# Optimization experiments

Measured on AMD Instinct MI355X. Metric: run time of the kernel, lower is better.

## Reference

```python
import jax, jax.numpy as jnp
import numpy as np

F = 32          # fmap_size = (256 // 16) * 2
WIN = F // 8 - 1  # window = 3
HID = 160
HID4 = 640
N = 4096
Q = 16


def setup_inputs() -> dict:
    key = jax.random.key(0)
    ks = jax.random.split(key, 24)

    def lin(k, i, o):
        return jax.random.normal(k, (i, o), jnp.float32) * (1.0 / np.sqrt(i))

    return {
        "feature_pos": jax.random.normal(ks[0], (N, Q, HID), jnp.float32),
        "query_embedding": jax.random.normal(ks[1], (N, Q, HID), jnp.float32),
        "attn_matrix": jax.random.normal(ks[2], (N, Q, F * F), jnp.float32),
        "ws1": lin(ks[3], HID, HID4), "bs1": jnp.zeros((HID4,), jnp.float32),
        "ws2": lin(ks[4], HID4, HID4), "bs2": jnp.zeros((HID4,), jnp.float32),
        "ws3": lin(ks[5], HID4, HID4), "bs3": jnp.zeros((HID4,), jnp.float32),
        "ws4": lin(ks[6], HID4, 1), "bs4": jnp.zeros((1,), jnp.float32),
        "wp1": lin(ks[7], HID, HID4), "bp1": jnp.zeros((HID4,), jnp.float32),
        "wp2": lin(ks[8], HID4, HID4), "bp2": jnp.zeros((HID4,), jnp.float32),
        "wp3": lin(ks[9], HID4, HID4), "bp3": jnp.zeros((HID4,), jnp.float32),
        "wp4": lin(ks[10], HID4, 4), "bp4": jnp.zeros((4,), jnp.float32),
    }


def _mlp(x, w1, b1, w2, b2, w3, b3, w4, b4):
    h = jax.nn.relu(x @ w1 + b1)
    h = jax.nn.relu(h @ w2 + b2)
    h = jax.nn.relu(h @ w3 + b3)
    return h @ w4 + b4


def _gauss_blur3(x):
    # torchvision GaussianBlur(3, sigma=1.0): separable 3-tap, reflect padding
    e = np.exp(-0.5)
    k = jnp.asarray([e, 1.0, e], jnp.float32) / np.float32(1.0 + 2.0 * e)
    xp = jnp.pad(x, ((0, 0), (1, 1), (0, 0)), mode="reflect")
    x = k[0] * xp[:, :-2] + k[1] * xp[:, 1:-1] + k[2] * xp[:, 2:]
    xp = jnp.pad(x, ((0, 0), (0, 0), (1, 1)), mode="reflect")
    return k[0] * xp[:, :, :-2] + k[1] * xp[:, :, 1:-1] + k[2] * xp[:, :, 2:]


def _process_attnmap(am):
    # am: [N, F, F]
    n = am.shape[0]
    ab = _gauss_blur3(am)
    ab = (ab - ab.mean(axis=(1, 2), keepdims=True)) / jnp.std(ab, axis=(1, 2), keepdims=True, ddof=1)
    idx = jnp.argmax(ab.reshape(n, -1), axis=1)
    px = (idx % F).astype(jnp.int32)
    py = (idx // F).astype(jnp.int32)
    # vectorized windowed mean of clamped sigmoid (masked instead of per-sample slicing)
    s = jnp.clip(jax.nn.sigmoid(am), 1e-4, 1.0 - 1e-4)
    pos = jnp.arange(F)
    colmask = ((pos[None, :] >= jnp.maximum(0, px - WIN)[:, None]) &
               (pos[None, :] < jnp.minimum(F, px + WIN)[:, None])).astype(s.dtype)  # [N,F]
    rowmask = ((pos[None, :] >= jnp.maximum(0, py - WIN)[:, None]) &
               (pos[None, :] < jnp.minimum(F, py + WIN)[:, None])).astype(s.dtype)
    colsum = s.sum(axis=1)  # [N,F] sum over rows -> per-column totals
    rowsum = s.sum(axis=2)  # [N,F] sum over cols -> per-row totals
    tempx = (colsum * colmask).sum(axis=1) / (F * colmask.sum(axis=1))
    tempy = (rowsum * rowmask).sum(axis=1) / (F * rowmask.sum(axis=1))
    prepos = jnp.stack([px, py], axis=1).astype(jnp.float32)          # [N,2]
    presize = jnp.stack([tempx, tempy], axis=1) * np.float32(F)        # [N,2]
    return prepos, presize


def reference(feature_pos, query_embedding, attn_matrix,
              ws1, bs1, ws2, bs2, ws3, bs3, ws4, bs4,
              wp1, bp1, wp2, bp2, wp3, bp3, wp4, bp4):
    n = query_embedding.shape[0]
    qe = query_embedding.mean(axis=1)   # [N, HID]
    fp = feature_pos.mean(axis=1)       # [N, HID]
    am = attn_matrix.mean(axis=1).reshape(n, F, F)
    score = _mlp(qe, ws1, bs1, ws2, bs2, ws3, bs3, ws4, bs4).reshape(n)
    bbox_info = _mlp(fp, wp1, bp1, wp2, bp2, wp3, bp3, wp4, bp4)  # [N,4]
    sizeoffset = jnp.clip(bbox_info[:, :2], -2.0, 2.0)
    posoffset = jnp.clip(bbox_info[:, 2:], -2.0, 2.0)
    prepos, presize = _process_attnmap(am)
    xy = (prepos + posoffset) / np.float32(F)
    wh = (presize + sizeoffset) / np.float32(F)
    xy = xy - 0.5 * wh  # predict_center
    bbox = jnp.concatenate([xy, wh], axis=1)
    return bbox, score
```

## Files before the change

kernel.cpp:

```cpp
#include <hip/hip_runtime.h>
#include <hip/hip_bf16.h>
#include <stdint.h>

#define HID 160
#define HID4 640
#define FDIM 32
#define NPIX 1024

#define GK0 0.27406862f
#define GK1 0.45186276f

typedef __attribute__((ext_vector_type(8))) short short8;
typedef __attribute__((ext_vector_type(4))) float f32x4;

__device__ __forceinline__ ushort f2b(float f) {
  union { float f; uint32_t u; } v; v.f = f;
  uint32_t u = v.u;
  u += 0x7fffu + ((u >> 16) & 1u);
  return (ushort)(u >> 16);
}
__device__ __forceinline__ float b2f(ushort s) {
  union { uint32_t u; float f; } v; v.u = ((uint32_t)s) << 16;
  return v.f;
}

__device__ __forceinline__ void gload16(const ushort* g, ushort* l) {
  __builtin_amdgcn_global_load_lds(
      (const __attribute__((address_space(1))) void*)g,
      (__attribute__((address_space(3))) void*)l, 16, 0, 0);
}

struct AttnSM {
  float am[FDIM][FDIM + 1];
  float tmp[FDIM][FDIM + 1];
  float bl[FDIM][FDIM + 1];
  float rowsum[FDIM], colsum[FDIM];
  float redv[4];
  int redi[4];
};

union GemmSM {
  struct {
    ushort la[2][4096];
    ushort lb[2][4096];
  } g;
  AttnSM a;
};

__device__ void attn_block(AttnSM& sm, const float* __restrict__ attn,
                           float* __restrict__ pp, int n) {
  const int tid = threadIdx.x;
  const float* base = attn + (size_t)n * (16 * NPIX);
  float4 a = make_float4(0.f, 0.f, 0.f, 0.f);
#pragma unroll
  for (int q = 0; q < 16; ++q) {
    float4 v = *(const float4*)(base + q * NPIX + tid * 4);
    a.x += v.x; a.y += v.y; a.z += v.z; a.w += v.w;
  }
  {
    const int f0 = tid * 4;
    const int r = f0 >> 5, c = f0 & 31;
    sm.am[r][c + 0] = a.x * 0.0625f;
    sm.am[r][c + 1] = a.y * 0.0625f;
    sm.am[r][c + 2] = a.z * 0.0625f;
    sm.am[r][c + 3] = a.w * 0.0625f;
  }
  __syncthreads();
  for (int f = tid; f < NPIX; f += 256) {
    int r = f >> 5, c = f & 31;
    int rm = (r == 0) ? 1 : r - 1;
    int rp = (r == 31) ? 30 : r + 1;
    sm.tmp[r][c] = GK0 * sm.am[rm][c] + GK1 * sm.am[r][c] + GK0 * sm.am[rp][c];
  }
  __syncthreads();
  for (int f = tid; f < NPIX; f += 256) {
    int r = f >> 5, c = f & 31;
    int cm = (c == 0) ? 1 : c - 1;
    int cp = (c == 31) ? 30 : c + 1;
    sm.bl[r][c] = GK0 * sm.tmp[r][cm] + GK1 * sm.tmp[r][c] + GK0 * sm.tmp[r][cp];
  }
  __syncthreads();
  float bv = -1e30f; int bi = 0;
  for (int f = tid; f < NPIX; f += 256) {
    float v = sm.bl[f >> 5][f & 31];
    if (v > bv || (v == bv && f < bi)) { bv = v; bi = f; }
  }
  for (int off = 32; off > 0; off >>= 1) {
    float ov = __shfl_down(bv, off);
    int oi = __shfl_down(bi, off);
    if (ov > bv || (ov == bv && oi < bi)) { bv = ov; bi = oi; }
  }
  if ((tid & 63) == 0) { sm.redv[tid >> 6] = bv; sm.redi[tid >> 6] = bi; }
  for (int f = tid; f < NPIX; f += 256) {
    int r = f >> 5, c = f & 31;
    float s = 1.f / (1.f + expf(-sm.am[r][c]));
    sm.tmp[r][c] = fminf(fmaxf(s, 1e-4f), 0.9999f);
  }
  __syncthreads();
  if (tid < 32) {
    float s = 0.f;
    for (int c = 0; c < 32; ++c) s += sm.tmp[tid][c];
    sm.rowsum[tid] = s;
  } else if (tid < 64) {
    int c = tid - 32;
    float s = 0.f;
    for (int r = 0; r < 32; ++r) s += sm.tmp[r][c];
    sm.colsum[c] = s;
  }
  __syncthreads();
  if (tid == 0) {
    float bestv = sm.redv[0]; int besti = sm.redi[0];
    for (int w = 1; w < 4; ++w)
      if (sm.redv[w] > bestv || (sm.redv[w] == bestv && sm.redi[w] < besti)) {
        bestv = sm.redv[w]; besti = sm.redi[w];
      }
    int px = besti & 31, py = besti >> 5;
    int c0 = max(0, px - 3), c1 = min(32, px + 3);
    float sx = 0.f;
    for (int c = c0; c < c1; ++c) sx += sm.colsum[c];
    float psx = (sx / (32.f * (float)(c1 - c0))) * 32.f;
    int r0 = max(0, py - 3), r1 = min(32, py + 3);
    float sy = 0.f;
    for (int r = r0; r < r1; ++r) sy += sm.rowsum[r];
    float psy = (sy / (32.f * (float)(r1 - r0))) * 32.f;
    pp[n * 4 + 0] = (float)px;
    pp[n * 4 + 1] = (float)py;
    pp[n * 4 + 2] = psx;
    pp[n * 4 + 3] = psy;
  }
}

template <int K>
__global__ __launch_bounds__(256) void gemm_attn(
    const ushort* __restrict__ A0, const ushort* __restrict__ A1,
    const ushort* __restrict__ W0, const ushort* __restrict__ W1,
    const float* __restrict__ B0, const float* __restrict__ B1,
    ushort* __restrict__ O0, ushort* __restrict__ O1,
    const float* __restrict__ attn, float* __restrict__ pp,
    int attn_base, int n_gemm) {
  __shared__ GemmSM sm;
  const int tid = threadIdx.x;

  if ((int)blockIdx.x >= n_gemm) {
    attn_block(sm.a, attn, pp, attn_base + (int)blockIdx.x - n_gemm);
    return;
  }

  const int bid = blockIdx.x;
  const int half = n_gemm >> 1;
  const int chain = bid >= half;
  const int r = chain ? bid - half : bid;
  const int bn = (r % 5) * 128;
  const int bm = (r / 5) * 128;
  const ushort* A = chain ? A1 : A0;
  const ushort* W = chain ? W1 : W0;
  const float* bias = chain ? B1 : B0;
  ushort* O = chain ? O1 : O0;

  const int lane = tid & 63;
  const int wid = tid >> 6;
  const int wr = (wid >> 1) * 64;
  const int wc = (wid & 1) * 64;
  const int l15 = lane & 15;
  const int kq = (lane >> 4) * 8;

  const int rstage = tid >> 2;
  const int cstage = (tid & 3) * 8;
  const int ldsbase = wid * 512;

  const size_t arow0 = (size_t)(bm + rstage) * K + cstage;
  const size_t arow1 = (size_t)(bm + 64 + rstage) * K + cstage;
  const size_t wrow0 = (size_t)(bn + rstage) * K + cstage;
  const size_t wrow1 = (size_t)(bn + 64 + rstage) * K + cstage;

  gload16(A + arow0, &sm.g.la[0][0] + ldsbase);
  gload16(W + wrow0, &sm.g.lb[0][0] + ldsbase);
  gload16(A + arow1, &sm.g.la[0][2048] + ldsbase);
  gload16(W + wrow1, &sm.g.lb[0][2048] + ldsbase);

  constexpr int NT = K / 32;
  f32x4 acc[4][4] = {};
  for (int t = 0; t < NT; ++t) {
    const int cur = t & 1;
    if (t + 1 < NT) {
      const int k1 = (t + 1) * 32;
      const int nxt = cur ^ 1;
      gload16(A + arow0 + k1, &sm.g.la[nxt][0] + ldsbase);
      gload16(W + wrow0 + k1, &sm.g.lb[nxt][0] + ldsbase);
      gload16(A + arow1 + k1, &sm.g.la[nxt][2048] + ldsbase);
      gload16(W + wrow1 + k1, &sm.g.lb[nxt][2048] + ldsbase);
      asm volatile("s_waitcnt vmcnt(4)" ::: "memory");
    } else {
      asm volatile("s_waitcnt vmcnt(0)" ::: "memory");
    }
    __builtin_amdgcn_s_barrier();

    const ushort* lac = &sm.g.la[cur][0];
    const ushort* lbc = &sm.g.lb[cur][0];
    short8 af[4], bf[4];
#pragma unroll
    for (int i = 0; i < 4; ++i) {
      af[i] = *(const short8*)(lac + (wr + i * 16 + l15) * 32 + kq);
      bf[i] = *(const short8*)(lbc + (wc + i * 16 + l15) * 32 + kq);
    }
#pragma unroll
    for (int mi = 0; mi < 4; ++mi)
#pragma unroll
      for (int nj = 0; nj < 4; ++nj)
        acc[mi][nj] = __builtin_amdgcn_mfma_f32_16x16x32_bf16(af[mi], bf[nj], acc[mi][nj], 0, 0, 0);

    __builtin_amdgcn_s_barrier();
  }

#pragma unroll
  for (int nj = 0; nj < 4; ++nj) {
    const int col = bn + wc + nj * 16 + l15;
    const float bcol = bias[col];
#pragma unroll
    for (int mi = 0; mi < 4; ++mi) {
      const int rbase = bm + wr + mi * 16 + (lane >> 4) * 4;
#pragma unroll
      for (int b = 0; b < 4; ++b) {
        float v = acc[mi][nj][b] + bcol;
        O[(size_t)(rbase + b) * HID4 + col] = f2b(fmaxf(v, 0.f));
      }
    }
  }
}

__global__ __launch_bounds__(256) void prep_kernel(
    const float* __restrict__ qemb, const float* __restrict__ fpos,
    ushort* __restrict__ qe_b, ushort* __restrict__ fp_b,
    const float* __restrict__ ws1, ushort* __restrict__ wts1,
    const float* __restrict__ wp1, ushort* __restrict__ wtp1,
    const float* __restrict__ ws2, ushort* __restrict__ wts2,
    const float* __restrict__ wp2, ushort* __restrict__ wtp2,
    const float* __restrict__ ws3, ushort* __restrict__ wts3,
    const float* __restrict__ wp3, ushort* __restrict__ wtp3,
    int n_mean_blocks, int total) {
  __shared__ float t[32][33];
  const int tid = threadIdx.x;
  const int bid = blockIdx.x;

  if (bid < n_mean_blocks) {
    int idx = bid * 256 + tid;
    const int pairs = total >> 1;
    const float* src; ushort* dst; int i;
    if (idx < pairs) { src = qemb; dst = qe_b; i = idx; }
    else             { src = fpos; dst = fp_b; i = idx - pairs; }
    int nn = i / (HID / 2);
    int h = (i - nn * (HID / 2)) * 2;
    const float* p = src + (size_t)nn * (16 * HID) + h;
    float sx = 0.f, sy = 0.f;
#pragma unroll
    for (int q = 0; q < 16; ++q) {
      float2 v = *(const float2*)(p + q * HID);
      sx += v.x; sy += v.y;
    }
    ushort2 o;
    o.x = f2b(sx * 0.0625f);
    o.y = f2b(sy * 0.0625f);
    *(ushort2*)(dst + (size_t)nn * HID + h) = o;
    return;
  }

  int r = bid - n_mean_blocks;
  const float* in; ushort* out; int K;
  if (r < 100)       { in = ws1; out = wts1; K = HID; }
  else if (r < 200)  { in = wp1; out = wtp1; K = HID; r -= 100; }
  else if (r < 600)  { in = ws2; out = wts2; K = HID4; r -= 200; }
  else if (r < 1000) { in = wp2; out = wtp2; K = HID4; r -= 600; }
  else if (r < 1400) { in = ws3; out = wts3; K = HID4; r -= 1000; }
  else               { in = wp3; out = wtp3; K = HID4; r -= 1400; }
  const int bx = (r % 20) * 32;
  const int by = (r / 20) * 32;
  const int lx = tid & 31;
  const int ly = tid >> 5;
#pragma unroll
  for (int i = 0; i < 4; ++i)
    t[ly + i * 8][lx] = in[(size_t)(by + ly + i * 8) * HID4 + bx + lx];
  __syncthreads();
#pragma unroll
  for (int i = 0; i < 4; ++i)
    out[(size_t)(bx + ly + i * 8) * K + by + lx] = f2b(t[lx][ly + i * 8]);
}

__global__ __launch_bounds__(256) void final_kernel(
    const ushort* __restrict__ hs, const ushort* __restrict__ hp,
    const float* __restrict__ ws4, const float* __restrict__ bs4,
    const float* __restrict__ wp4, const float* __restrict__ bp4,
    const float* __restrict__ pp, float* __restrict__ out, int N) {
  const int wid = threadIdx.x >> 6;
  const int lane = threadIdx.x & 63;
  const int n = blockIdx.x * 4 + wid;
  if (n >= N) return;
  const ushort* hsr = hs + (size_t)n * HID4;
  const ushort* hpr = hp + (size_t)n * HID4;
  float sc = 0.f, b0 = 0.f, b1 = 0.f, b2 = 0.f, b3 = 0.f;
  for (int j = lane; j < HID4; j += 64) {
    float h1 = b2f(hsr[j]);
    sc += h1 * ws4[j];
    float h2 = b2f(hpr[j]);
    b0 += h2 * wp4[j * 4 + 0];
    b1 += h2 * wp4[j * 4 + 1];
    b2 += h2 * wp4[j * 4 + 2];
    b3 += h2 * wp4[j * 4 + 3];
  }
  for (int off = 32; off > 0; off >>= 1) {
    sc += __shfl_down(sc, off);
    b0 += __shfl_down(b0, off);
    b1 += __shfl_down(b1, off);
    b2 += __shfl_down(b2, off);
    b3 += __shfl_down(b3, off);
  }
  if (lane == 0) {
    sc += bs4[0];
    b0 += bp4[0]; b1 += bp4[1]; b2 += bp4[2]; b3 += bp4[3];
    float so0 = fminf(fmaxf(b0, -2.f), 2.f);
    float so1 = fminf(fmaxf(b1, -2.f), 2.f);
    float po0 = fminf(fmaxf(b2, -2.f), 2.f);
    float po1 = fminf(fmaxf(b3, -2.f), 2.f);
    float px = pp[n * 4 + 0], py = pp[n * 4 + 1];
    float psx = pp[n * 4 + 2], psy = pp[n * 4 + 3];
    float wh0 = (psx + so0) * (1.f / 32.f);
    float wh1 = (psy + so1) * (1.f / 32.f);
    float xy0 = (px + po0) * (1.f / 32.f) - 0.5f * wh0;
    float xy1 = (py + po1) * (1.f / 32.f) - 0.5f * wh1;
    out[n * 4 + 0] = xy0;
    out[n * 4 + 1] = xy1;
    out[n * 4 + 2] = wh0;
    out[n * 4 + 3] = wh1;
    out[(size_t)4 * N + n] = sc;
  }
}

extern "C" void kernel_launch(void* const* d_in, const int* in_sizes, int n_in,
                              void* d_out, int out_size, void* d_ws, size_t ws_size,
                              hipStream_t stream) {
  const float* fpos = (const float*)d_in[0];
  const float* qemb = (const float*)d_in[1];
  const float* attn = (const float*)d_in[2];
  const float* ws1 = (const float*)d_in[3];
  const float* bs1 = (const float*)d_in[4];
  const float* ws2 = (const float*)d_in[5];
  const float* bs2 = (const float*)d_in[6];
  const float* ws3 = (const float*)d_in[7];
  const float* bs3 = (const float*)d_in[8];
  const float* ws4 = (const float*)d_in[9];
  const float* bs4 = (const float*)d_in[10];
  const float* wp1 = (const float*)d_in[11];
  const float* bp1 = (const float*)d_in[12];
  const float* wp2 = (const float*)d_in[13];
  const float* bp2 = (const float*)d_in[14];
  const float* wp3 = (const float*)d_in[15];
  const float* bp3 = (const float*)d_in[16];
  const float* wp4 = (const float*)d_in[17];
  const float* bp4 = (const float*)d_in[18];
  float* out = (float*)d_out;

  const int N = in_sizes[0] / (16 * HID);

  char* ws = (char*)d_ws;
  const size_t SZ_QE = (size_t)N * HID * 2;
  const size_t SZ_W1 = (size_t)HID4 * HID * 2;
  const size_t SZ_W2 = (size_t)HID4 * HID4 * 2;
  const size_t SZ_H  = (size_t)N * HID4 * 2;
  size_t off = 0;
  ushort* qe_b = (ushort*)(ws + off); off += SZ_QE;
  ushort* fp_b = (ushort*)(ws + off); off += SZ_QE;
  ushort* wts1 = (ushort*)(ws + off); off += SZ_W1;
  ushort* wtp1 = (ushort*)(ws + off); off += SZ_W1;
  ushort* wts2 = (ushort*)(ws + off); off += SZ_W2;
  ushort* wtp2 = (ushort*)(ws + off); off += SZ_W2;
  ushort* wts3 = (ushort*)(ws + off); off += SZ_W2;
  ushort* wtp3 = (ushort*)(ws + off); off += SZ_W2;
  ushort* hsA  = (ushort*)(ws + off); off += SZ_H;
  ushort* hsB  = (ushort*)(ws + off); off += SZ_H;
  ushort* hpA  = (ushort*)(ws + off); off += SZ_H;
  ushort* hpB  = (ushort*)(ws + off); off += SZ_H;
  float*  pp   = (float*)(ws + off);  off += (size_t)N * 4 * 4;

  const int total = N * HID;
  const int n_mean = (total + 255) / 256;
  const int n_trans = 1800;
  prep_kernel<<<n_mean + n_trans, 256, 0, stream>>>(
      qemb, fpos, qe_b, fp_b, ws1, wts1, wp1, wtp1, ws2, wts2, wp2, wtp2,
      ws3, wts3, wp3, wtp3, n_mean, total);

  const int n_gemm = 2 * (N / 128) * (HID4 / 128);

  const int a2 = (N * 29) / 100;
  const int a3 = a2;
  const int a1 = N - a2 - a3;

  gemm_attn<HID><<<n_gemm + a1, 256, 0, stream>>>(
      qe_b, fp_b, wts1, wtp1, bs1, bp1, hsA, hpA, attn, pp, 0, n_gemm);
  gemm_attn<HID4><<<n_gemm + a2, 256, 0, stream>>>(
      hsA, hpA, wts2, wtp2, bs2, bp2, hsB, hpB, attn, pp, a1, n_gemm);
  gemm_attn<HID4><<<n_gemm + a3, 256, 0, stream>>>(
      hsB, hpB, wts3, wtp3, bs3, bp3, hsA, hpA, attn, pp, a1 + a2, n_gemm);

  final_kernel<<<(N + 3) / 4, 256, 0, stream>>>(hsA, hpA, ws4, bs4, wp4, bp4, pp, out, N);
}
```

Before: 120.0 us.

## Split attention processing into mean and blur/argmax phases across kernels

Attention-map processing is split into two roles. A bandwidth-bound role averages the 16 queries and writes an intermediate mean map to workspace; these blocks are spread across the prep kernel and the first two GEMM launches. A compute role does the blur, argmax and window sums, and all of it is packed into the third GEMM launch. The aim is a better balance of memory-heavy and compute-heavy side work against the GEMMs, at the cost of an extra round trip through a 16 MB intermediate buffer.

```diff
diff --git a/kernel.cpp b/kernel.cpp
--- a/kernel.cpp
+++ b/kernel.cpp
@@ -47,23 +47,31 @@
   AttnSM a;
 };
 
-__device__ void attn_block(AttnSM& sm, const float* __restrict__ attn,
-                           float* __restrict__ pp, int n) {
+__device__ __forceinline__ void attn_mean_role(const float* __restrict__ attn,
+                                               float* __restrict__ amaps, int n) {
+  const int t = threadIdx.x;
+  const float* base = attn + (size_t)n * (16 * NPIX) + t * 4;
+  float4 a = make_float4(0.f, 0.f, 0.f, 0.f);
+#pragma unroll
+  for (int q = 0; q < 16; ++q) {
+    float4 v = *(const float4*)(base + q * NPIX);
+    a.x += v.x; a.y += v.y; a.z += v.z; a.w += v.w;
+  }
+  a.x *= 0.0625f; a.y *= 0.0625f; a.z *= 0.0625f; a.w *= 0.0625f;
+  *(float4*)(amaps + (size_t)n * NPIX + t * 4) = a;
+}
+
+__device__ void attn_process(AttnSM& sm, const float* __restrict__ amaps,
+                             float* __restrict__ pp, int n) {
   const int tid = threadIdx.x;
-  const float* base = attn + (size_t)n * (16 * NPIX);
-  float4 a = make_float4(0.f, 0.f, 0.f, 0.f);
-#pragma unroll
-  for (int q = 0; q < 16; ++q) {
-    float4 v = *(const float4*)(base + q * NPIX + tid * 4);
-    a.x += v.x; a.y += v.y; a.z += v.z; a.w += v.w;
-  }
   {
+    float4 a = *(const float4*)(amaps + (size_t)n * NPIX + tid * 4);
     const int f0 = tid * 4;
     const int r = f0 >> 5, c = f0 & 31;
-    sm.am[r][c + 0] = a.x * 0.0625f;
-    sm.am[r][c + 1] = a.y * 0.0625f;
-    sm.am[r][c + 2] = a.z * 0.0625f;
-    sm.am[r][c + 3] = a.w * 0.0625f;
+    sm.am[r][c + 0] = a.x;
+    sm.am[r][c + 1] = a.y;
+    sm.am[r][c + 2] = a.z;
+    sm.am[r][c + 3] = a.w;
   }
   __syncthreads();
   for (int f = tid; f < NPIX; f += 256) {
@@ -136,13 +144,15 @@
     const ushort* __restrict__ W0, const ushort* __restrict__ W1,
     const float* __restrict__ B0, const float* __restrict__ B1,
     ushort* __restrict__ O0, ushort* __restrict__ O1,
-    const float* __restrict__ attn, float* __restrict__ pp,
-    int attn_base, int n_gemm) {
+    const float* __restrict__ attn, float* __restrict__ amaps,
+    float* __restrict__ pp, int mode, int attn_base, int n_gemm) {
   __shared__ GemmSM sm;
   const int tid = threadIdx.x;
 
   if ((int)blockIdx.x >= n_gemm) {
-    attn_block(sm.a, attn, pp, attn_base + (int)blockIdx.x - n_gemm);
+    const int rb = (int)blockIdx.x - n_gemm;
+    if (mode == 0) attn_mean_role(attn, amaps, attn_base + rb);
+    else attn_process(sm.a, amaps, pp, attn_base + rb);
     return;
   }
 
@@ -237,7 +247,8 @@
     const float* __restrict__ wp2, ushort* __restrict__ wtp2,
     const float* __restrict__ ws3, ushort* __restrict__ wts3,
     const float* __restrict__ wp3, ushort* __restrict__ wtp3,
-    int n_mean_blocks, int total) {
+    const float* __restrict__ attn, float* __restrict__ amaps,
+    int n_mean_blocks, int n_trans_blocks, int total) {
   __shared__ float t[32][33];
   const int tid = threadIdx.x;
   const int bid = blockIdx.x;
@@ -264,25 +275,30 @@
     return;
   }
 
-  int r = bid - n_mean_blocks;
-  const float* in; ushort* out; int K;
-  if (r < 100)       { in = ws1; out = wts1; K = HID; }
-  else if (r < 200)  { in = wp1; out = wtp1; K = HID; r -= 100; }
-  else if (r < 600)  { in = ws2; out = wts2; K = HID4; r -= 200; }
-  else if (r < 1000) { in = wp2; out = wtp2; K = HID4; r -= 600; }
-  else if (r < 1400) { in = ws3; out = wts3; K = HID4; r -= 1000; }
-  else               { in = wp3; out = wtp3; K = HID4; r -= 1400; }
-  const int bx = (r % 20) * 32;
-  const int by = (r / 20) * 32;
-  const int lx = tid & 31;
-  const int ly = tid >> 5;
-#pragma unroll
-  for (int i = 0; i < 4; ++i)
-    t[ly + i * 8][lx] = in[(size_t)(by + ly + i * 8) * HID4 + bx + lx];
-  __syncthreads();
-#pragma unroll
-  for (int i = 0; i < 4; ++i)
-    out[(size_t)(bx + ly + i * 8) * K + by + lx] = f2b(t[lx][ly + i * 8]);
+  if (bid < n_mean_blocks + n_trans_blocks) {
+    int r = bid - n_mean_blocks;
+    const float* in; ushort* out; int K;
+    if (r < 100)       { in = ws1; out = wts1; K = HID; }
+    else if (r < 200)  { in = wp1; out = wtp1; K = HID; r -= 100; }
+    else if (r < 600)  { in = ws2; out = wts2; K = HID4; r -= 200; }
+    else if (r < 1000) { in = wp2; out = wtp2; K = HID4; r -= 600; }
+    else if (r < 1400) { in = ws3; out = wts3; K = HID4; r -= 1000; }
+    else               { in = wp3; out = wtp3; K = HID4; r -= 1400; }
+    const int bx = (r % 20) * 32;
+    const int by = (r / 20) * 32;
+    const int lx = tid & 31;
+    const int ly = tid >> 5;
+#pragma unroll
+    for (int i = 0; i < 4; ++i)
+      t[ly + i * 8][lx] = in[(size_t)(by + ly + i * 8) * HID4 + bx + lx];
+    __syncthreads();
+#pragma unroll
+    for (int i = 0; i < 4; ++i)
+      out[(size_t)(bx + ly + i * 8) * K + by + lx] = f2b(t[lx][ly + i * 8]);
+    return;
+  }
+
+  attn_mean_role(attn, amaps, bid - n_mean_blocks - n_trans_blocks);
 }
 
 __global__ __launch_bounds__(256) void final_kernel(
@@ -379,26 +395,29 @@
   ushort* hpA  = (ushort*)(ws + off); off += SZ_H;
   ushort* hpB  = (ushort*)(ws + off); off += SZ_H;
   float*  pp   = (float*)(ws + off);  off += (size_t)N * 4 * 4;
+  float*  amaps = (float*)(ws + off); off += (size_t)N * NPIX * 4;
+
+  const int s1 = 560;
+  const int s2 = 2240;
 
   const int total = N * HID;
   const int n_mean = (total + 255) / 256;
   const int n_trans = 1800;
-  prep_kernel<<<n_mean + n_trans, 256, 0, stream>>>(
+  prep_kernel<<<n_mean + n_trans + s1, 256, 0, stream>>>(
       qemb, fpos, qe_b, fp_b, ws1, wts1, wp1, wtp1, ws2, wts2, wp2, wtp2,
-      ws3, wts3, wp3, wtp3, n_mean, total);
+      ws3, wts3, wp3, wtp3, attn, amaps, n_mean, n_trans, total);
 
   const int n_gemm = 2 * (N / 128) * (HID4 / 128);
 
-  const int a2 = (N * 29) / 100;
-  const int a3 = a2;
-  const int a1 = N - a2 - a3;
-
-  gemm_attn<HID><<<n_gemm + a1, 256, 0, stream>>>(
-      qe_b, fp_b, wts1, wtp1, bs1, bp1, hsA, hpA, attn, pp, 0, n_gemm);
-  gemm_attn<HID4><<<n_gemm + a2, 256, 0, stream>>>(
-      hsA, hpA, wts2, wtp2, bs2, bp2, hsB, hpB, attn, pp, a1, n_gemm);
-  gemm_attn<HID4><<<n_gemm + a3, 256, 0, stream>>>(
-      hsB, hpB, wts3, wtp3, bs3, bp3, hsA, hpA, attn, pp, a1 + a2, n_gemm);
+  gemm_attn<HID><<<n_gemm + (s2 - s1), 256, 0, stream>>>(
+      qe_b, fp_b, wts1, wtp1, bs1, bp1, hsA, hpA,
+      attn, amaps, pp, 0, s1, n_gemm);
+  gemm_attn<HID4><<<n_gemm + (N - s2), 256, 0, stream>>>(
+      hsA, hpA, wts2, wtp2, bs2, bp2, hsB, hpB,
+      attn, amaps, pp, 0, s2, n_gemm);
+  gemm_attn<HID4><<<n_gemm + N, 256, 0, stream>>>(
+      hsB, hpB, wts3, wtp3, bs3, bp3, hsA, hpA,
+      attn, amaps, pp, 1, 0, n_gemm);
 
   final_kernel<<<(N + 3) / 4, 256, 0, stream>>>(hsA, hpA, ws4, bs4, wp4, bp4, pp, out, N);
 }
```

Measured after the change: 136.5 us. 1.14x slower.
